# Performance work log

Measured on AMD Instinct MI355X. Metric: run time of the kernel, lower is better.

The kernel has to match this reference:

```python
import jax, jax.numpy as jnp
import numpy as np

L, H, E, V, N, VOCAB = 6, 16, 1024, 32, 4096, 32000
D_SQRT = float(np.sqrt(V))


def _positions(n, e):
    # Faithful to source: exponent uses d = max_context_size (n), and the
    # ternary is INSIDE sin(): even i -> sin(x), odd i -> sin(cos(x)).
    pos = np.arange(n, dtype=np.float64)[:, None]
    i = np.arange(e, dtype=np.float64)[None, :]
    x = pos / (10000.0 ** (2.0 * i / n))
    arr = np.where((np.arange(e)[None, :] % 2) == 0, np.sin(x), np.sin(np.cos(x)))
    return jnp.asarray(arr, dtype=jnp.float32)


def setup_inputs() -> dict:
    key = jax.random.key(0)
    ks = jax.random.split(key, 10)
    context = jax.random.randint(ks[0], (N,), 0, VOCAB)
    table = jax.random.normal(ks[1], (VOCAB, E), dtype=jnp.float32)
    pos = _positions(N, E)
    # torch.rand-style uniform weights, scaled small for numerical sanity
    Wq = jax.random.uniform(ks[2], (L, H, E, V), dtype=jnp.float32) * 0.05
    Wk = jax.random.uniform(ks[3], (L, H, E, V), dtype=jnp.float32) * 0.05
    Wv = jax.random.uniform(ks[4], (L, H, E, V), dtype=jnp.float32) * 0.05
    Wo = jax.random.uniform(ks[5], (L, H * V, E), dtype=jnp.float32) * 0.05
    W1 = jax.random.normal(ks[6], (L, E, 2 * E), dtype=jnp.float32) * 0.02
    b1 = jnp.zeros((L, 2 * E), dtype=jnp.float32)
    W2 = jax.random.normal(ks[7], (L, 2 * E, E), dtype=jnp.float32) * 0.02
    b2 = jnp.zeros((L, E), dtype=jnp.float32)
    return {"context": context, "table": table, "pos": pos, "Wq": Wq, "Wk": Wk,
            "Wv": Wv, "Wo": Wo, "W1": W1, "b1": b1, "W2": W2, "b2": b2}


def _layernorm(x):
    # source LayerNorm: mean/std over dim=1, unbiased std (ddof=1), no eps
    m = jnp.mean(x, axis=1, keepdims=True)
    s = jnp.std(x, axis=1, ddof=1, keepdims=True)
    return (x - m) / s


def _block(z, p):
    wq, wk, wv, wo, w1, bb1, w2, bb2 = p
    q = jnp.einsum('ne,hev->hnv', z, wq)
    k = jnp.einsum('ne,hev->hnv', z, wk)
    v = jnp.einsum('ne,hev->hnv', z, wv)
    att = jax.nn.softmax(jnp.einsum('hnv,hmv->hnm', q, k) / D_SQRT, axis=-1)
    o = jnp.einsum('hnm,hmv->nhv', att, v).reshape(z.shape[0], -1)  # concat heads on dim 1
    an = _layernorm(z + o @ wo)
    ff = jax.nn.leaky_relu(an @ w1 + bb1, 0.01) @ w2 + bb2
    return _layernorm(an + ff), None


def reference(context, table, pos, Wq, Wk, Wv, Wo, W1, b1, W2, b2):
    z0 = table[context] + pos  # [N, E]
    z, _ = jax.lax.scan(_block, z0, (Wq, Wk, Wv, Wo, W1, b1, W2, b2))
    return z
```

## Files before the change

kernel.cpp:

```cpp
#include <hip/hip_runtime.h>
#include <hip/hip_bf16.h>

typedef _Float16 f16;
typedef __attribute__((ext_vector_type(8))) _Float16 f16x8;
typedef __attribute__((ext_vector_type(4))) float f4v;

constexpr int NSEQ = 4096;
constexpr int EMB  = 1024;
constexpr int NH   = 16;
constexpr int HD   = 32;
constexpr int NL   = 6;
constexpr int HV   = NH * HD;
constexpr int FF   = 2 * EMB;
constexpr int QKVW = 3 * HV;

#define BARRIER_LGKM() do { \
    asm volatile("s_waitcnt lgkmcnt(0)" ::: "memory"); \
    __builtin_amdgcn_s_barrier(); \
    asm volatile("" ::: "memory"); } while (0)

#define GLDS16(gp, lp) __builtin_amdgcn_global_load_lds( \
    (const __attribute__((address_space(1))) void*)(const void*)(gp), \
    (__attribute__((address_space(3))) void*)(void*)(lp), 16, 0, 0)

__device__ __forceinline__ unsigned pk2h(float a, float b) {
  auto h = __builtin_amdgcn_cvt_pkrtz(a, b);
  unsigned d; __builtin_memcpy(&d, &h, 4);
  return d;
}

__global__ __launch_bounds__(256) void embed_kernel(const int* __restrict__ ctx,
    const float* __restrict__ table, const float* __restrict__ pos,
    float* __restrict__ z, f16* __restrict__ zh){
  int t = blockIdx.x * 256 + threadIdx.x;
  int n = t >> 8;
  int e = (t & 255) << 2;
  float4 a = *reinterpret_cast<const float4*>(table + (size_t)ctx[n] * EMB + e);
  float4 b = *reinterpret_cast<const float4*>(pos   + (size_t)n * EMB + e);
  float4 r = {a.x + b.x, a.y + b.y, a.z + b.z, a.w + b.w};
  *reinterpret_cast<float4*>(z + (size_t)n * EMB + e) = r;
  f16 o[4] = {(f16)r.x, (f16)r.y, (f16)r.z, (f16)r.w};
  uint2 u; __builtin_memcpy(&u, o, 8);
  *reinterpret_cast<uint2*>(zh + (size_t)n * EMB + e) = u;
}

__global__ __launch_bounds__(256) void convT_kernel(const float* __restrict__ in,
    f16* __restrict__ out, int K, int N, long sInZ, long sOutZ){
  __shared__ float t[32][33];
  in  += (size_t)blockIdx.z * sInZ;
  out += (size_t)blockIdx.z * sOutZ;
  int k0 = blockIdx.x * 32, n0 = blockIdx.y * 32;
  int r = threadIdx.x >> 5, c = threadIdx.x & 31;
  #pragma unroll
  for (int i = 0; i < 4; i++)
    t[r + i*8][c] = in[(size_t)(k0 + r + i*8) * N + n0 + c];
  __syncthreads();
  #pragma unroll
  for (int i = 0; i < 4; i++)
    out[(size_t)(n0 + r + i*8) * K + k0 + c] = (f16)t[c][r + i*8];
}

template<typename CT>
__global__ __launch_bounds__(256) void gemm_mfma(
    const f16* __restrict__ A, const f16* __restrict__ Bt, CT* C,
    const float* __restrict__ bias, const float* res,
    int K, int Nc, int leaky)
{
  __shared__ f16 Ash[128 * 32];
  __shared__ f16 Bsh[128 * 32];
  int tid = threadIdx.x;
  int lane = tid & 63, w = tid >> 6;
  int wm = w & 1, wn = w >> 1;
  int l16 = lane & 15, quad = lane >> 4;
  int row0 = blockIdx.y * 128, col0 = blockIdx.x * 128;

  f4v acc[4][4];
  #pragma unroll
  for (int i = 0; i < 4; i++)
    #pragma unroll
    for (int j = 0; j < 4; j++) acc[i][j] = {0.f, 0.f, 0.f, 0.f};

  int srow = lane >> 2;
  int scol = (lane & 3) * 8;
  const f16* gA0 = A  + (size_t)(row0 + w*32      + srow) * K + scol;
  const f16* gA1 = A  + (size_t)(row0 + w*32 + 16 + srow) * K + scol;
  const f16* gB0 = Bt + (size_t)(col0 + w*32      + srow) * K + scol;
  const f16* gB1 = Bt + (size_t)(col0 + w*32 + 16 + srow) * K + scol;
  f16* lA0 = Ash + (w*2    ) * 512;
  f16* lA1 = Ash + (w*2 + 1) * 512;
  f16* lB0 = Bsh + (w*2    ) * 512;
  f16* lB1 = Bsh + (w*2 + 1) * 512;

  for (int k0 = 0; k0 < K; k0 += 32) {
    __syncthreads();
    GLDS16(gA0 + k0, lA0);
    GLDS16(gA1 + k0, lA1);
    GLDS16(gB0 + k0, lB0);
    GLDS16(gB1 + k0, lB1);
    __syncthreads();
    f16x8 af[4], bf[4];
    #pragma unroll
    for (int mt = 0; mt < 4; mt++)
      af[mt] = *reinterpret_cast<const f16x8*>(&Ash[(wm*64 + mt*16 + l16) * 32 + quad*8]);
    #pragma unroll
    for (int nt = 0; nt < 4; nt++)
      bf[nt] = *reinterpret_cast<const f16x8*>(&Bsh[(wn*64 + nt*16 + l16) * 32 + quad*8]);
    #pragma unroll
    for (int mt = 0; mt < 4; mt++)
      #pragma unroll
      for (int nt = 0; nt < 4; nt++)
        acc[mt][nt] = __builtin_amdgcn_mfma_f32_16x16x32_f16(af[mt], bf[nt], acc[mt][nt], 0, 0, 0);
  }

  #pragma unroll
  for (int mt = 0; mt < 4; mt++) {
    #pragma unroll
    for (int nt = 0; nt < 4; nt++) {
      int ccol = col0 + wn*64 + nt*16 + l16;
      float bv = bias ? bias[ccol] : 0.f;
      #pragma unroll
      for (int reg = 0; reg < 4; reg++) {
        int crow = row0 + wm*64 + mt*16 + quad*4 + reg;
        float v = acc[mt][nt][reg] + bv;
        if (leaky) v = v > 0.f ? v : 0.01f * v;
        if (res)   v += res[(size_t)crow * Nc + ccol];
        if constexpr (sizeof(CT) == 2) C[(size_t)crow * Nc + ccol] = (f16)v;
        else                           C[(size_t)crow * Nc + ccol] = v;
      }
    }
  }
}

__global__ __launch_bounds__(256) void attn_mfma(const f16* __restrict__ qkv,
    f16* __restrict__ O)
{
  __shared__ f16 Ks[128][40];
  __shared__ f16 Vt[32][136];
  __shared__ f16 Ps[4][16][136];
  int tid = threadIdx.x;
  int lane = tid & 63, w = tid >> 6;
  int l16 = lane & 15, quad = lane >> 4;
  int h = blockIdx.y;
  int q0 = blockIdx.x * 64 + w * 16;
  const float sc = 0.17677669529663687f * 1.4426950408889634f;

  f16x8 qf;
  {
    union { uint4 u; f16 e[8]; } qc;
    qc.u = *reinterpret_cast<const uint4*>(
        qkv + (size_t)(q0 + l16) * QKVW + h * HD + quad * 8);
    #pragma unroll
    for (int i = 0; i < 8; i++) qc.e[i] = (f16)((float)qc.e[i] * sc);
    __builtin_memcpy(&qf, qc.e, 16);
  }

  float m_ = -1e30f, lsum = 0.f;
  f4v oaccT[2];
  oaccT[0] = {0.f,0.f,0.f,0.f}; oaccT[1] = {0.f,0.f,0.f,0.f};

  int ksrow = tid >> 1, ksc = (tid & 1) * 16;
  int vkp = tid & 63, vdg = tid >> 6;

  uint4 ka, kb, va, vb;
  {
    const f16* kp0 = qkv + (size_t)ksrow * QKVW + HV + h * HD + ksc;
    ka = *reinterpret_cast<const uint4*>(kp0);
    kb = *reinterpret_cast<const uint4*>(kp0 + 8);
    const f16* vp0 = qkv + (size_t)(2 * vkp) * QKVW + 2 * HV + h * HD + vdg * 8;
    va = *reinterpret_cast<const uint4*>(vp0);
    vb = *reinterpret_cast<const uint4*>(vp0 + QKVW);
  }

  for (int kt = 0; kt < NSEQ; kt += 128) {
    BARRIER_LGKM();
    *reinterpret_cast<uint4*>(&Ks[ksrow][ksc])     = ka;
    *reinterpret_cast<uint4*>(&Ks[ksrow][ksc + 8]) = kb;
    {
      union { uint4 u; f16 e[8]; } c0, c1; c0.u = va; c1.u = vb;
      #pragma unroll
      for (int i = 0; i < 8; i++) {
        f16 pr[2] = {c0.e[i], c1.e[i]};
        unsigned d; __builtin_memcpy(&d, pr, 4);
        *reinterpret_cast<unsigned*>(&Vt[vdg * 8 + i][2 * vkp]) = d;
      }
    }
    {
      int ktn = (kt + 128) & (NSEQ - 1);
      const f16* kp0 = qkv + (size_t)(ktn + ksrow) * QKVW + HV + h * HD + ksc;
      ka = *reinterpret_cast<const uint4*>(kp0);
      kb = *reinterpret_cast<const uint4*>(kp0 + 8);
      const f16* vp0 = qkv + (size_t)(ktn + 2 * vkp) * QKVW + 2 * HV + h * HD + vdg * 8;
      va = *reinterpret_cast<const uint4*>(vp0);
      vb = *reinterpret_cast<const uint4*>(vp0 + QKVW);
    }
    BARRIER_LGKM();

    f4v s4[8];
    __builtin_amdgcn_s_setprio(1);
    #pragma unroll
    for (int t = 0; t < 8; t++) {
      f16x8 kf = *reinterpret_cast<const f16x8*>(&Ks[t * 16 + l16][quad * 8]);
      s4[t] = __builtin_amdgcn_mfma_f32_16x16x32_f16(kf, qf, (f4v){0.f,0.f,0.f,0.f}, 0, 0, 0);
    }
    __builtin_amdgcn_s_setprio(0);

    float tmt[8];
    #pragma unroll
    for (int t = 0; t < 8; t++)
      tmt[t] = fmaxf(fmaxf(fmaxf(s4[t][0], s4[t][1]), s4[t][2]), s4[t][3]);
    float m01 = fmaxf(tmt[0], tmt[1]), m23 = fmaxf(tmt[2], tmt[3]);
    float m45 = fmaxf(tmt[4], tmt[5]), m67 = fmaxf(tmt[6], tmt[7]);
    float tm = fmaxf(fmaxf(m01, m23), fmaxf(m45, m67));
    tm = fmaxf(tm, __shfl_xor(tm, 16));
    tm = fmaxf(tm, __shfl_xor(tm, 32));
    if (!__all(tm <= m_)) {
      float mN = fmaxf(m_, tm);
      float corr = __builtin_amdgcn_exp2f(m_ - mN);
      m_ = mN;
      lsum *= corr;
      #pragma unroll
      for (int vt = 0; vt < 2; vt++)
        #pragma unroll
        for (int r = 0; r < 4; r++) oaccT[vt][r] *= corr;
    }
    float ls = 0.f;
    #pragma unroll
    for (int t = 0; t < 8; t++) {
      float p0 = __builtin_amdgcn_exp2f(s4[t][0] - m_);
      float p1 = __builtin_amdgcn_exp2f(s4[t][1] - m_);
      float p2 = __builtin_amdgcn_exp2f(s4[t][2] - m_);
      float p3 = __builtin_amdgcn_exp2f(s4[t][3] - m_);
      ls += (p0 + p1) + (p2 + p3);
      uint2 d;
      d.x = pk2h(p0, p1);
      d.y = pk2h(p2, p3);
      *reinterpret_cast<uint2*>(&Ps[w][l16][t * 16 + quad * 4]) = d;
    }
    lsum += ls;
    __builtin_amdgcn_s_setprio(1);
    #pragma unroll
    for (int kc = 0; kc < 4; kc++) {
      f16x8 pf = *reinterpret_cast<const f16x8*>(&Ps[w][l16][kc * 32 + quad * 8]);
      #pragma unroll
      for (int vt = 0; vt < 2; vt++) {
        f16x8 vf = *reinterpret_cast<const f16x8*>(&Vt[vt * 16 + l16][kc * 32 + quad * 8]);
        oaccT[vt] = __builtin_amdgcn_mfma_f32_16x16x32_f16(vf, pf, oaccT[vt], 0, 0, 0);
      }
    }
    __builtin_amdgcn_s_setprio(0);
  }
  lsum += __shfl_xor(lsum, 16);
  lsum += __shfl_xor(lsum, 32);
  float inv = 1.f / lsum;
  #pragma unroll
  for (int vt = 0; vt < 2; vt++) {
    f16 ob[4];
    #pragma unroll
    for (int r = 0; r < 4; r++) ob[r] = (f16)(oaccT[vt][r] * inv);
    uint2 u; __builtin_memcpy(&u, ob, 8);
    *reinterpret_cast<uint2*>(
        O + (size_t)(q0 + l16) * HV + h * HD + vt * 16 + quad * 4) = u;
  }
}

__global__ __launch_bounds__(256) void ln_kernel(const float* in, float* out,
                                                 f16* __restrict__ outh){
  __shared__ float sm[8];
  int row = blockIdx.x, tid = threadIdx.x;
  float4 x = reinterpret_cast<const float4*>(in + (size_t)row * EMB)[tid];
  float s = x.x + x.y + x.z + x.w;
  #pragma unroll
  for (int o = 32; o > 0; o >>= 1) s += __shfl_down(s, o);
  int wid = tid >> 6, lane = tid & 63;
  if (lane == 0) sm[wid] = s;
  __syncthreads();
  float mean = (sm[0] + sm[1] + sm[2] + sm[3]) * (1.f / EMB);
  float dx = x.x - mean, dy = x.y - mean, dz = x.z - mean, dw = x.w - mean;
  float qs = dx*dx + dy*dy + dz*dz + dw*dw;
  #pragma unroll
  for (int o = 32; o > 0; o >>= 1) qs += __shfl_down(qs, o);
  if (lane == 0) sm[4 + wid] = qs;
  __syncthreads();
  float var = (sm[4] + sm[5] + sm[6] + sm[7]) * (1.f / (EMB - 1));
  float inv = rsqrtf(var);
  float4 y = {dx * inv, dy * inv, dz * inv, dw * inv};
  reinterpret_cast<float4*>(out + (size_t)row * EMB)[tid] = y;
  f16 o4[4] = {(f16)y.x, (f16)y.y, (f16)y.z, (f16)y.w};
  uint2 u; __builtin_memcpy(&u, o4, 8);
  reinterpret_cast<uint2*>(outh + (size_t)row * EMB)[tid] = u;
}

extern "C" void kernel_launch(void* const* d_in, const int* in_sizes, int n_in,
                              void* d_out, int out_size, void* d_ws, size_t ws_size,
                              hipStream_t stream)
{
  const int*   ctx   = (const int*)d_in[0];
  const float* table = (const float*)d_in[1];
  const float* pos   = (const float*)d_in[2];
  const float* Wq    = (const float*)d_in[3];
  const float* Wk    = (const float*)d_in[4];
  const float* Wv    = (const float*)d_in[5];
  const float* Wo    = (const float*)d_in[6];
  const float* W1    = (const float*)d_in[7];
  const float* b1    = (const float*)d_in[8];
  const float* W2    = (const float*)d_in[9];
  const float* b2    = (const float*)d_in[10];

  float* z = (float*)d_out;

  char* ws = (char*)d_ws;
  const size_t MB = 1u << 20;
  float* an   = (float*)(ws);
  f16*   anh  = (f16*)  (ws + 16 * MB);
  f16*   zh   = (f16*)  (ws + 24 * MB);
  f16*   qkvh = (f16*)  (ws + 32 * MB);
  f16*   Oh   = (f16*)  (ws + 44 * MB);
  f16*   h1h  = (f16*)  (ws + 32 * MB);
  f16*   wbuf = (f16*)  (ws + 48 * MB);

  embed_kernel<<<NSEQ * EMB / 4 / 256, 256, 0, stream>>>(ctx, table, pos, z, zh);

  for (int l = 0; l < NL; l++) {
    const float* wq  = Wq + (size_t)l * NH * EMB * HD;
    const float* wk  = Wk + (size_t)l * NH * EMB * HD;
    const float* wv  = Wv + (size_t)l * NH * EMB * HD;
    const float* wo  = Wo + (size_t)l * HV * EMB;
    const float* w1  = W1 + (size_t)l * EMB * FF;
    const float* bb1 = b1 + (size_t)l * FF;
    const float* w2  = W2 + (size_t)l * FF * EMB;
    const float* bb2 = b2 + (size_t)l * EMB;

    convT_kernel<<<dim3(EMB/32, 1, NH), 256, 0, stream>>>(
        wq, wbuf + (size_t)0 * HV * EMB, EMB, HD, (long)EMB * HD, (long)HD * EMB);
    convT_kernel<<<dim3(EMB/32, 1, NH), 256, 0, stream>>>(
        wk, wbuf + (size_t)1 * HV * EMB, EMB, HD, (long)EMB * HD, (long)HD * EMB);
    convT_kernel<<<dim3(EMB/32, 1, NH), 256, 0, stream>>>(
        wv, wbuf + (size_t)2 * HV * EMB, EMB, HD, (long)EMB * HD, (long)HD * EMB);
    gemm_mfma<f16><<<dim3(QKVW/128, NSEQ/128), 256, 0, stream>>>(
        zh, wbuf, qkvh, nullptr, nullptr, EMB, QKVW, 0);

    attn_mfma<<<dim3(NSEQ/64, NH), 256, 0, stream>>>(qkvh, Oh);

    convT_kernel<<<dim3(HV/32, EMB/32, 1), 256, 0, stream>>>(
        wo, wbuf, HV, EMB, 0, 0);
    gemm_mfma<float><<<dim3(EMB/128, NSEQ/128), 256, 0, stream>>>(
        Oh, wbuf, z, nullptr, z, HV, EMB, 0);
    ln_kernel<<<NSEQ, 256, 0, stream>>>(z, an, anh);

    convT_kernel<<<dim3(EMB/32, FF/32, 1), 256, 0, stream>>>(
        w1, wbuf, EMB, FF, 0, 0);
    gemm_mfma<f16><<<dim3(FF/128, NSEQ/128), 256, 0, stream>>>(
        anh, wbuf, h1h, bb1, nullptr, EMB, FF, 1);
    convT_kernel<<<dim3(FF/32, EMB/32, 1), 256, 0, stream>>>(
        w2, wbuf, FF, EMB, 0, 0);
    gemm_mfma<float><<<dim3(EMB/128, NSEQ/128), 256, 0, stream>>>(
        h1h, wbuf, z, bb2, an, FF, EMB, 0);
    ln_kernel<<<NSEQ, 256, 0, stream>>>(z, z, zh);
  }
}
```

Before: 1.962 ms.

## Rewrite attention with 32x32 MFMA, register P exchange, double-buffered K/V

```diff
diff --git a/kernel.cpp b/kernel.cpp
--- a/kernel.cpp
+++ b/kernel.cpp
@@ -4,6 +4,7 @@
 typedef _Float16 f16;
 typedef __attribute__((ext_vector_type(8))) _Float16 f16x8;
 typedef __attribute__((ext_vector_type(4))) float f4v;
+typedef __attribute__((ext_vector_type(16))) float f32x16;
 
 constexpr int NSEQ = 4096;
 constexpr int EMB  = 1024;
@@ -13,11 +14,6 @@
 constexpr int HV   = NH * HD;
 constexpr int FF   = 2 * EMB;
 constexpr int QKVW = 3 * HV;
-
-#define BARRIER_LGKM() do { \
-    asm volatile("s_waitcnt lgkmcnt(0)" ::: "memory"); \
-    __builtin_amdgcn_s_barrier(); \
-    asm volatile("" ::: "memory"); } while (0)
 
 #define GLDS16(gp, lp) __builtin_amdgcn_global_load_lds( \
     (const __attribute__((address_space(1))) void*)(const void*)(gp), \
@@ -131,135 +127,156 @@
   }
 }
 
-__global__ __launch_bounds__(256) void attn_mfma(const f16* __restrict__ qkv,
+__global__ __launch_bounds__(128) void attn_mfma(const f16* __restrict__ qkv,
     f16* __restrict__ O)
 {
-  __shared__ f16 Ks[128][40];
-  __shared__ f16 Vt[32][136];
-  __shared__ f16 Ps[4][16][136];
+  __shared__ f16 Ks[2][128][40];
+  __shared__ f16 Vt[2][32][136];
   int tid = threadIdx.x;
   int lane = tid & 63, w = tid >> 6;
-  int l16 = lane & 15, quad = lane >> 4;
-  int h = blockIdx.y;
-  int q0 = blockIdx.x * 64 + w * 16;
+  int l31 = lane & 31, h = lane >> 5;
+  int hd = blockIdx.y;
+  int q0 = blockIdx.x * 64 + w * 32;
   const float sc = 0.17677669529663687f * 1.4426950408889634f;
 
-  f16x8 qf;
+  f16x8 qf0, qf1;
   {
-    union { uint4 u; f16 e[8]; } qc;
-    qc.u = *reinterpret_cast<const uint4*>(
-        qkv + (size_t)(q0 + l16) * QKVW + h * HD + quad * 8);
-    #pragma unroll
-    for (int i = 0; i < 8; i++) qc.e[i] = (f16)((float)qc.e[i] * sc);
-    __builtin_memcpy(&qf, qc.e, 16);
+    const f16* qp = qkv + (size_t)(q0 + l31) * QKVW + hd * HD + h * 8;
+    union { uint4 u; f16 e[8]; } a, b;
+    a.u = *reinterpret_cast<const uint4*>(qp);
+    b.u = *reinterpret_cast<const uint4*>(qp + 16);
+    #pragma unroll
+    for (int i = 0; i < 8; i++) {
+      a.e[i] = (f16)((float)a.e[i] * sc);
+      b.e[i] = (f16)((float)b.e[i] * sc);
+    }
+    __builtin_memcpy(&qf0, a.e, 16);
+    __builtin_memcpy(&qf1, b.e, 16);
   }
 
   float m_ = -1e30f, lsum = 0.f;
-  f4v oaccT[2];
-  oaccT[0] = {0.f,0.f,0.f,0.f}; oaccT[1] = {0.f,0.f,0.f,0.f};
-
-  int ksrow = tid >> 1, ksc = (tid & 1) * 16;
-  int vkp = tid & 63, vdg = tid >> 6;
-
-  uint4 ka, kb, va, vb;
-  {
-    const f16* kp0 = qkv + (size_t)ksrow * QKVW + HV + h * HD + ksc;
-    ka = *reinterpret_cast<const uint4*>(kp0);
-    kb = *reinterpret_cast<const uint4*>(kp0 + 8);
-    const f16* vp0 = qkv + (size_t)(2 * vkp) * QKVW + 2 * HV + h * HD + vdg * 8;
-    va = *reinterpret_cast<const uint4*>(vp0);
-    vb = *reinterpret_cast<const uint4*>(vp0 + QKVW);
-  }
+  f32x16 oaccA, oaccB, zz;
+  #pragma unroll
+  for (int i = 0; i < 16; i++) { oaccA[i] = 0.f; oaccB[i] = 0.f; zz[i] = 0.f; }
+
+  int vkp = tid & 63;
+  uint4 kr0, kr1, kr2, kr3, vr0, vr1, vr2, vr3;
+
+  auto LOADT = [&](int kt) {
+    const f16* kp = qkv + (size_t)(kt + tid) * QKVW + HV + hd * HD;
+    const uint4* kq = reinterpret_cast<const uint4*>(kp);
+    kr0 = kq[0]; kr1 = kq[1]; kr2 = kq[2]; kr3 = kq[3];
+    const f16* vp = qkv + (size_t)(kt + 2*vkp) * QKVW + 2*HV + hd * HD + w * 16;
+    vr0 = *reinterpret_cast<const uint4*>(vp);
+    vr1 = *reinterpret_cast<const uint4*>(vp + QKVW);
+    vr2 = *reinterpret_cast<const uint4*>(vp + 8);
+    vr3 = *reinterpret_cast<const uint4*>(vp + QKVW + 8);
+  };
+  auto WRITET = [&](int b) {
+    *reinterpret_cast<uint4*>(&Ks[b][tid][0])  = kr0;
+    *reinterpret_cast<uint4*>(&Ks[b][tid][8])  = kr1;
+    *reinterpret_cast<uint4*>(&Ks[b][tid][16]) = kr2;
+    *reinterpret_cast<uint4*>(&Ks[b][tid][24]) = kr3;
+    union { uint4 u; f16 e[8]; } c0, c1, c2, c3;
+    c0.u = vr0; c1.u = vr1; c2.u = vr2; c3.u = vr3;
+    #pragma unroll
+    for (int i = 0; i < 8; i++) {
+      f16 p0[2] = {c0.e[i], c1.e[i]};
+      unsigned d0; __builtin_memcpy(&d0, p0, 4);
+      *reinterpret_cast<unsigned*>(&Vt[b][w*16 + i][2*vkp]) = d0;
+      f16 p1[2] = {c2.e[i], c3.e[i]};
+      unsigned d1; __builtin_memcpy(&d1, p1, 4);
+      *reinterpret_cast<unsigned*>(&Vt[b][w*16 + 8 + i][2*vkp]) = d1;
+    }
+  };
+
+  LOADT(0);
+  WRITET(0);
+  __syncthreads();
+  int cur = 0;
 
   for (int kt = 0; kt < NSEQ; kt += 128) {
-    BARRIER_LGKM();
-    *reinterpret_cast<uint4*>(&Ks[ksrow][ksc])     = ka;
-    *reinterpret_cast<uint4*>(&Ks[ksrow][ksc + 8]) = kb;
-    {
-      union { uint4 u; f16 e[8]; } c0, c1; c0.u = va; c1.u = vb;
-      #pragma unroll
-      for (int i = 0; i < 8; i++) {
-        f16 pr[2] = {c0.e[i], c1.e[i]};
-        unsigned d; __builtin_memcpy(&d, pr, 4);
-        *reinterpret_cast<unsigned*>(&Vt[vdg * 8 + i][2 * vkp]) = d;
-      }
-    }
-    {
-      int ktn = (kt + 128) & (NSEQ - 1);
-      const f16* kp0 = qkv + (size_t)(ktn + ksrow) * QKVW + HV + h * HD + ksc;
-      ka = *reinterpret_cast<const uint4*>(kp0);
-      kb = *reinterpret_cast<const uint4*>(kp0 + 8);
-      const f16* vp0 = qkv + (size_t)(ktn + 2 * vkp) * QKVW + 2 * HV + h * HD + vdg * 8;
-      va = *reinterpret_cast<const uint4*>(vp0);
-      vb = *reinterpret_cast<const uint4*>(vp0 + QKVW);
-    }
-    BARRIER_LGKM();
-
-    f4v s4[8];
+    LOADT((kt + 128) & (NSEQ - 1));
+
+    f32x16 s0, s1, s2, s3;
     __builtin_amdgcn_s_setprio(1);
-    #pragma unroll
-    for (int t = 0; t < 8; t++) {
-      f16x8 kf = *reinterpret_cast<const f16x8*>(&Ks[t * 16 + l16][quad * 8]);
-      s4[t] = __builtin_amdgcn_mfma_f32_16x16x32_f16(kf, qf, (f4v){0.f,0.f,0.f,0.f}, 0, 0, 0);
-    }
+    #define SCHUNK(sv, c) { \
+      f16x8 a0 = *reinterpret_cast<const f16x8*>(&Ks[cur][(c)*32 + l31][h*8]); \
+      f16x8 a1 = *reinterpret_cast<const f16x8*>(&Ks[cur][(c)*32 + l31][16 + h*8]); \
+      sv = __builtin_amdgcn_mfma_f32_32x32x16_f16(a0, qf0, zz, 0, 0, 0); \
+      sv = __builtin_amdgcn_mfma_f32_32x32x16_f16(a1, qf1, sv, 0, 0, 0); }
+    SCHUNK(s0, 0) SCHUNK(s1, 1) SCHUNK(s2, 2) SCHUNK(s3, 3)
+    #undef SCHUNK
     __builtin_amdgcn_s_setprio(0);
 
-    float tmt[8];
-    #pragma unroll
-    for (int t = 0; t < 8; t++)
-      tmt[t] = fmaxf(fmaxf(fmaxf(s4[t][0], s4[t][1]), s4[t][2]), s4[t][3]);
-    float m01 = fmaxf(tmt[0], tmt[1]), m23 = fmaxf(tmt[2], tmt[3]);
-    float m45 = fmaxf(tmt[4], tmt[5]), m67 = fmaxf(tmt[6], tmt[7]);
-    float tm = fmaxf(fmaxf(m01, m23), fmaxf(m45, m67));
-    tm = fmaxf(tm, __shfl_xor(tm, 16));
+    auto cmax = [](const f32x16& s) {
+      float a = fmaxf(fmaxf(s[0], s[1]),   fmaxf(s[2], s[3]));
+      float b = fmaxf(fmaxf(s[4], s[5]),   fmaxf(s[6], s[7]));
+      float c = fmaxf(fmaxf(s[8], s[9]),   fmaxf(s[10], s[11]));
+      float d = fmaxf(fmaxf(s[12], s[13]), fmaxf(s[14], s[15]));
+      return fmaxf(fmaxf(a, b), fmaxf(c, d));
+    };
+    float tm = fmaxf(fmaxf(cmax(s0), cmax(s1)), fmaxf(cmax(s2), cmax(s3)));
     tm = fmaxf(tm, __shfl_xor(tm, 32));
     if (!__all(tm <= m_)) {
       float mN = fmaxf(m_, tm);
       float corr = __builtin_amdgcn_exp2f(m_ - mN);
-      m_ = mN;
-      lsum *= corr;
+      m_ = mN; lsum *= corr;
       #pragma unroll
-      for (int vt = 0; vt < 2; vt++)
-        #pragma unroll
-        for (int r = 0; r < 4; r++) oaccT[vt][r] *= corr;
+      for (int i = 0; i < 16; i++) { oaccA[i] *= corr; oaccB[i] *= corr; }
     }
+
     float ls = 0.f;
-    #pragma unroll
-    for (int t = 0; t < 8; t++) {
-      float p0 = __builtin_amdgcn_exp2f(s4[t][0] - m_);
-      float p1 = __builtin_amdgcn_exp2f(s4[t][1] - m_);
-      float p2 = __builtin_amdgcn_exp2f(s4[t][2] - m_);
-      float p3 = __builtin_amdgcn_exp2f(s4[t][3] - m_);
-      ls += (p0 + p1) + (p2 + p3);
-      uint2 d;
-      d.x = pk2h(p0, p1);
-      d.y = pk2h(p2, p3);
-      *reinterpret_cast<uint2*>(&Ps[w][l16][t * 16 + quad * 4]) = d;
-    }
+    #define PVCHUNK(sv, c, oacc) { \
+      float pv[16]; \
+      _Pragma("unroll") \
+      for (int r_ = 0; r_ < 16; r_++) { \
+        pv[r_] = __builtin_amdgcn_exp2f(sv[r_] - m_); ls += pv[r_]; } \
+      unsigned d00 = pk2h(pv[0],  pv[1]),  d01 = pk2h(pv[2],  pv[3]);  \
+      unsigned d10 = pk2h(pv[4],  pv[5]),  d11 = pk2h(pv[6],  pv[7]);  \
+      unsigned d20 = pk2h(pv[8],  pv[9]),  d21 = pk2h(pv[10], pv[11]); \
+      unsigned d30 = pk2h(pv[12], pv[13]), d31 = pk2h(pv[14], pv[15]); \
+      unsigned rxA0 = (unsigned)__shfl_xor((int)(h ? d00 : d10), 32); \
+      unsigned rxA1 = (unsigned)__shfl_xor((int)(h ? d01 : d11), 32); \
+      unsigned rxB0 = (unsigned)__shfl_xor((int)(h ? d20 : d30), 32); \
+      unsigned rxB1 = (unsigned)__shfl_xor((int)(h ? d21 : d31), 32); \
+      unsigned o00 = h ? d10 : d00, o01 = h ? d11 : d01; \
+      unsigned o10 = h ? d30 : d20, o11 = h ? d31 : d21; \
+      unsigned fr0[4] = { h ? rxA0 : o00, h ? rxA1 : o01, \
+                          h ? o00 : rxA0, h ? o01 : rxA1 }; \
+      unsigned fr1[4] = { h ? rxB0 : o10, h ? rxB1 : o11, \
+                          h ? o10 : rxB0, h ? o11 : rxB1 }; \
+      f16x8 pb0, pb1; \
+      __builtin_memcpy(&pb0, fr0, 16); __builtin_memcpy(&pb1, fr1, 16); \
+      f16x8 vf0 = *reinterpret_cast<const f16x8*>(&Vt[cur][l31][(c)*32 + h*8]); \
+      f16x8 vf1 = *reinterpret_cast<const f16x8*>(&Vt[cur][l31][(c)*32 + 16 + h*8]); \
+      __builtin_amdgcn_s_setprio(1); \
+      oacc = __builtin_amdgcn_mfma_f32_32x32x16_f16(vf0, pb0, oacc, 0, 0, 0); \
+      oacc = __builtin_amdgcn_mfma_f32_32x32x16_f16(vf1, pb1, oacc, 0, 0, 0); \
+      __builtin_amdgcn_s_setprio(0); }
+    PVCHUNK(s0, 0, oaccA)
+    PVCHUNK(s1, 1, oaccB)
+    PVCHUNK(s2, 2, oaccA)
+    PVCHUNK(s3, 3, oaccB)
+    #undef PVCHUNK
     lsum += ls;
-    __builtin_amdgcn_s_setprio(1);
-    #pragma unroll
-    for (int kc = 0; kc < 4; kc++) {
-      f16x8 pf = *reinterpret_cast<const f16x8*>(&Ps[w][l16][kc * 32 + quad * 8]);
-      #pragma unroll
-      for (int vt = 0; vt < 2; vt++) {
-        f16x8 vf = *reinterpret_cast<const f16x8*>(&Vt[vt * 16 + l16][kc * 32 + quad * 8]);
-        oaccT[vt] = __builtin_amdgcn_mfma_f32_16x16x32_f16(vf, pf, oaccT[vt], 0, 0, 0);
-      }
-    }
-    __builtin_amdgcn_s_setprio(0);
-  }
-  lsum += __shfl_xor(lsum, 16);
+
+    if (kt + 128 < NSEQ) WRITET(cur ^ 1);
+    __syncthreads();
+    cur ^= 1;
+  }
+
   lsum += __shfl_xor(lsum, 32);
   float inv = 1.f / lsum;
-  #pragma unroll
-  for (int vt = 0; vt < 2; vt++) {
+  f16* op = O + (size_t)(q0 + l31) * HV + hd * HD;
+  #pragma unroll
+  for (int g = 0; g < 4; g++) {
     f16 ob[4];
     #pragma unroll
-    for (int r = 0; r < 4; r++) ob[r] = (f16)(oaccT[vt][r] * inv);
+    for (int r = 0; r < 4; r++)
+      ob[r] = (f16)((oaccA[4*g + r] + oaccB[4*g + r]) * inv);
     uint2 u; __builtin_memcpy(&u, ob, 8);
-    *reinterpret_cast<uint2*>(
-        O + (size_t)(q0 + l16) * HV + h * HD + vt * 16 + quad * 4) = u;
+    *reinterpret_cast<uint2*>(op + 8*g + 4*h) = u;
   }
 }
 
@@ -339,7 +356,7 @@
     gemm_mfma<f16><<<dim3(QKVW/128, NSEQ/128), 256, 0, stream>>>(
         zh, wbuf, qkvh, nullptr, nullptr, EMB, QKVW, 0);
 
-    attn_mfma<<<dim3(NSEQ/64, NH), 256, 0, stream>>>(qkvh, Oh);
+    attn_mfma<<<dim3(NSEQ/64, NH), 128, 0, stream>>>(qkvh, Oh);
 
     convT_kernel<<<dim3(HV/32, EMB/32, 1), 256, 0, stream>>>(
         wo, wbuf, HV, EMB, 0, 0);
```

After: 2.017 ms. 2.8% more time.
